# Kernel tuning notes

Measured on AMD Instinct MI355X. Metric: run time of the kernel, lower is better.

The kernel has to match this reference:

```python
import jax, jax.numpy as jnp
import numpy as np

B, L, N = 64, 64, 32           # programs, statement trees per program, nodes per tree
V, E, C, H, OUT = 100000, 128, 128, 100, 104
MAX_DEPTH = 10


def setup_inputs() -> dict:
    key = jax.random.key(0)
    ks = jax.random.split(key, 14)
    rng = np.random.default_rng(0)
    num_trees = B * L
    T = num_trees * N
    # random trees: parent index < node index, depth capped at MAX_DEPTH
    par = np.zeros((num_trees, N), np.int64)
    lev = np.zeros((num_trees, N), np.int64)
    for i in range(1, N):
        p = rng.integers(0, i, size=num_trees)
        pl = lev[np.arange(num_trees), p]
        too_deep = pl + 1 > MAX_DEPTH
        p = np.where(too_deep, 0, p)
        lev[:, i] = np.where(too_deep, 1, pl + 1)
        par[:, i] = p
    base = (np.arange(num_trees) * N)[:, None]
    parent = jnp.asarray((par + base).reshape(-1))          # global parent index
    level = jnp.asarray(lev.reshape(-1))
    tree_id = jnp.asarray(np.repeat(np.arange(num_trees), N))
    node_ids = jax.random.randint(ks[0], (T,), 0, V)
    r = lambda k, shape, s=0.05: (jax.random.normal(k, shape) * s).astype(jnp.float32)
    return {
        'node_ids': node_ids, 'parent': parent, 'level': level, 'tree_id': tree_id,
        'emb': r(ks[1], (V, E), 1.0),
        'W_lin': r(ks[2], (E, C)), 'b_lin': r(ks[3], (C,)),
        'w_ih_f': r(ks[4], (3 * H, C)), 'w_hh_f': r(ks[5], (3 * H, H)),
        'b_ih_f': r(ks[6], (3 * H,)), 'b_hh_f': r(ks[7], (3 * H,)),
        'w_ih_b': r(ks[8], (3 * H, C)), 'w_hh_b': r(ks[9], (3 * H, H)),
        'b_ih_b': r(ks[10], (3 * H,)), 'b_hh_b': r(ks[11], (3 * H,)),
        'fc_w': r(ks[12], (2 * H, OUT)), 'fc_b': r(ks[13], (OUT,)),
    }


def _run_gru(xs, wih, whh, bih, bhh, reverse):
    # xs: [L, B, C]; torch GRU gate math
    def step(hprev, x):
        gi = x @ wih.T + bih
        gh = hprev @ whh.T + bhh
        ir, iz, inn = jnp.split(gi, 3, axis=-1)
        hr, hz, hn = jnp.split(gh, 3, axis=-1)
        rg = jax.nn.sigmoid(ir + hr)
        zg = jax.nn.sigmoid(iz + hz)
        ng = jnp.tanh(inn + rg * hn)
        hnew = (1.0 - zg) * ng + zg * hprev
        return hnew, hnew
    h0 = jnp.zeros((xs.shape[1], whh.shape[1]), xs.dtype)
    _, out = jax.lax.scan(step, h0, xs, reverse=reverse)
    return out  # [L, B, H]


def _forward(node_ids, parent, level, tree_id, emb, W_lin, b_lin,
             w_ih_f, w_hh_f, b_ih_f, b_hh_f, w_ih_b, w_hh_b, b_ih_b, b_hh_b,
             fc_w, fc_b):
    # per-node: h = W*emb(id) + b, then child-sum bottom-up by depth level
    h = emb[node_ids] @ W_lin + b_lin            # [T, C]
    for d in range(MAX_DEPTH, 0, -1):
        contrib = jnp.where((level == d)[:, None], h, 0.0)
        h = h.at[parent].add(contrib)
    # per-tree max pool over all node hidden states -> statement vectors
    stmt = jax.ops.segment_max(h, tree_id, num_segments=B * L)  # [B*L, C]
    xs = stmt.reshape(B, L, C).transpose(1, 0, 2)               # [L, B, C]
    out_f = _run_gru(xs, w_ih_f, w_hh_f, b_ih_f, b_hh_f, reverse=False)
    out_b = _run_gru(xs, w_ih_b, w_hh_b, b_ih_b, b_hh_b, reverse=True)
    gru_out = jnp.concatenate([out_f, out_b], axis=-1)          # [L, B, 2H]
    pooled = gru_out.max(axis=0)                                # [B, 2H]
    return pooled @ fc_w + fc_b                                 # [B, OUT]


def reference(node_ids, parent, level, tree_id, emb, W_lin, b_lin,
              w_ih_f, w_hh_f, b_ih_f, b_hh_f, w_ih_b, w_hh_b, b_ih_b, b_hh_b,
              fc_w, fc_b):
    return _forward(node_ids, parent, level, tree_id, emb, W_lin, b_lin,
                    w_ih_f, w_hh_f, b_ih_f, b_hh_f, w_ih_b, w_hh_b, b_ih_b, b_hh_b,
                    fc_w, fc_b)
```

## Files before the change

kernel.cpp:

```cpp
#include <hip/hip_runtime.h>

typedef _Float16 half8 __attribute__((ext_vector_type(8)));
typedef float f32x4 __attribute__((ext_vector_type(4)));
typedef float f32x16 __attribute__((ext_vector_type(16)));

union H8 { half8 h; float4 f; };
union F4 { float4 f; f32x4 v; };

#define EDIM 128
#define CDIM 128
#define HDIM 100
#define ODIM 104

#define OFF_WFRAG  0u
#define OFF_WIH    32768u
#define OFF_WHH    229376u
#define OFF_BIASP  401408u
#define OFF_BHHN   404480u
#define OFF_STMT   405504u
#define OFF_GI     1454080u
#define OFF_POOL   14036992u

__device__ inline f32x4 zero4() { f32x4 z = {0.f, 0.f, 0.f, 0.f}; return z; }

__device__ inline float fast_exp2(float x) {
  float r; asm("v_exp_f32 %0, %1" : "=v"(r) : "v"(x)); return r;
}
__device__ inline float fast_rcp(float x) {
  float r; asm("v_rcp_f32 %0, %1" : "=v"(r) : "v"(x)); return r;
}
__device__ inline float sigmoid_f(float x) {
  return fast_rcp(1.f + fast_exp2(x * -1.44269504f));
}
__device__ inline float tanh_f(float x) {
  float e = fast_exp2(x * 2.88539008f);
  return fmaf(fast_rcp(1.f + e), -2.f, 1.f);
}

#define HSWZ(row) ((((row) & 3) << 4) ^ (((row) & 12) << 3))

__global__ __launch_bounds__(256) void astnn_prep(
    const float* __restrict__ W_lin,
    const float* __restrict__ wihf, const float* __restrict__ whhf,
    const float* __restrict__ bihf, const float* __restrict__ bhhf,
    const float* __restrict__ wihb, const float* __restrict__ whhb,
    const float* __restrict__ bihb, const float* __restrict__ bhhb,
    _Float16* __restrict__ wfrag, _Float16* __restrict__ wihfrag,
    _Float16* __restrict__ whhfrag, float* __restrict__ biasP)
{
  int gid = blockIdx.x * 256 + threadIdx.x;
  if (gid < 2048) {
    int i = gid, l = i & 63, kc = (i >> 6) & 3, nt = i >> 8;
    int n = (nt << 4) + (l & 15);
    int kb = (kc << 5) + ((l >> 4) << 3);
#pragma unroll
    for (int e = 0; e < 8; e++)
      wfrag[i * 8 + e] = (_Float16)W_lin[(kb + e) * CDIM + n];
  } else if (gid < 14336) {
    int i = gid - 2048, l = i & 63, kc = (i >> 6) & 7;
    int rest = i >> 9, nt = rest % 12, d = rest / 12;
    const float* wih = d ? wihb : wihf;
    int n = (nt << 5) + (l & 31), s = n >> 7, j = n & 127;
    int kb = (kc << 4) + ((l >> 5) << 3);
#pragma unroll
    for (int e = 0; e < 8; e++) {
      float v = (j < HDIM) ? wih[(s * HDIM + j) * CDIM + (kb + e)] : 0.f;
      wihfrag[i * 8 + e] = (_Float16)v;
    }
  } else if (gid < 25088) {
    int i = gid - 14336, l = i & 63, kc = (i >> 6) & 3;
    int rest = i >> 8, nt = rest % 21, d = rest / 21;
    const float* whh = d ? whhb : whhf;
    const float* bhh = d ? bhhb : bhhf;
    int n = (nt << 4) + (l & 15), s = n / 112, j = n - 112 * s;
    int kb = (kc << 5) + ((l >> 4) << 3);
#pragma unroll
    for (int e = 0; e < 8; e++) {
      int k = kb + e;
      float v = 0.f;
      if (j < HDIM) {
        if (k < HDIM) v = whh[(s * HDIM + j) * HDIM + k];
        else if (k == HDIM && s == 2) v = bhh[2 * HDIM + j];
      }
      whhfrag[i * 8 + e] = (_Float16)v;
    }
  } else if (gid < 25856) {
    int i = gid - 25088, d = i / 384, col = i % 384, s = col >> 7, j = col & 127;
    const float* bih = d ? bihb : bihf;
    const float* bhh = d ? bhhb : bhhf;
    float v = 0.f;
    if (j < HDIM) { v = bih[s * HDIM + j]; if (s < 2) v += bhh[s * HDIM + j]; }
    biasP[i] = v;
  }
}

__global__ __launch_bounds__(256, 2) void astnn_tree(
    const int* __restrict__ node_ids, const int* __restrict__ parent,
    const float* __restrict__ emb, const float* __restrict__ b_lin,
    const _Float16* __restrict__ wfrag, _Float16* __restrict__ stmt)
{
  __shared__ _Float16 ldsW[16384];
  __shared__ _Float16 ldsA[16384];
  __shared__ int ldsPar[128];
  __shared__ unsigned ldsAnc[128];

  const int t = threadIdx.x, blk = blockIdx.x;
  const int w = t >> 6, l = t & 63;
  const int base = blk * 128;

  if (t < 128) ldsPar[t] = parent[base + t] & 31;

  {
    const float4* wsrc = (const float4*)wfrag;
#pragma unroll
    for (int i = 0; i < 8; i++) ((float4*)ldsW)[i * 256 + t] = wsrc[i * 256 + t];
  }

  {
    const int r = t >> 1, hf = t & 1;
    const int nid = node_ids[base + r];
    const float4* erow = (const float4*)(emb + (size_t)nid * EDIM) + hf * 16;
#pragma unroll
    for (int b2 = 0; b2 < 2; b2++) {
      float4 stage[8];
#pragma unroll
      for (int i = 0; i < 8; i++) stage[i] = erow[b2 * 8 + i];
#pragma unroll
      for (int c4 = 0; c4 < 4; c4++) {
        H8 u;
#pragma unroll
        for (int e = 0; e < 8; e++)
          u.h[e] = (_Float16)(((const float*)&stage[0])[c4 * 8 + e]);
        int c = b2 * 4 + c4;
        int addr = (r * 256 + hf * 128 + c * 16) ^ ((r & 7) << 4);
        *(float4*)((char*)ldsA + addr) = u.f;
      }
    }
  }
  __syncthreads();

  if (t < 128) {
    int tree = t >> 5;
    unsigned mask = 0;
    int cur = t & 31;
#pragma unroll
    for (int it = 0; it < 11; ++it) { mask |= (1u << cur); cur = ldsPar[tree * 32 + cur]; }
    ldsAnc[t] = mask;
  }
  __syncthreads();

  f32x4 acc[2][8];
#pragma unroll
  for (int mt = 0; mt < 2; mt++)
#pragma unroll
    for (int nt = 0; nt < 8; nt++) acc[mt][nt] = zero4();
#pragma unroll
  for (int kc = 0; kc < 4; kc++) {
    half8 af[2];
#pragma unroll
    for (int mt = 0; mt < 2; mt++) {
      int row = (w * 2 + mt) * 16 + (l & 15);
      int addr = (row * 256 + (kc << 6) + ((l >> 4) << 4)) ^ ((row & 7) << 4);
      af[mt] = *(const half8*)((const char*)ldsA + addr);
    }
#pragma unroll
    for (int nt = 0; nt < 8; nt++) {
      half8 bf = *(const half8*)&ldsW[(((nt << 2) | kc) * 64 + l) * 8];
      acc[0][nt] = __builtin_amdgcn_mfma_f32_16x16x32_f16(af[0], bf, acc[0][nt], 0, 0, 0);
      acc[1][nt] = __builtin_amdgcn_mfma_f32_16x16x32_f16(af[1], bf, acc[1][nt], 0, 0, 0);
    }
  }
  __syncthreads();

#pragma unroll
  for (int mt = 0; mt < 2; mt++) {
    const int Mt = w * 2 + mt, tree = Mt >> 1, kc2 = Mt & 1;
#pragma unroll
    for (int nt = 0; nt < 8; nt++) {
      const float bl = b_lin[nt * 16 + (l & 15)];
      const int nt2 = nt >> 1;
      const int ncol = ((nt & 1) << 4) + (l & 15);
#pragma unroll
      for (int reg = 0; reg < 4; reg++) {
        int rowrem = ((l >> 4) << 2) + reg;
        int l2 = ((rowrem >> 3) << 5) + ncol;
        int idx = (((((tree << 2) + nt2) << 1) + kc2) * 64 + l2) * 8 + (rowrem & 7);
        ldsA[idx] = (_Float16)(acc[mt][nt][reg] + bl);
      }
    }
  }
  __syncthreads();

  {
    const int tree = w;
    half8 ancf[2];
#pragma unroll
    for (int kc2 = 0; kc2 < 2; kc2++) {
      H8 u;
#pragma unroll
      for (int e = 0; e < 8; e++) {
        int n = (kc2 << 4) + ((l >> 5) << 3) + e;
        unsigned m = ldsAnc[(tree << 5) + n];
        u.h[e] = (_Float16)(float)((m >> (l & 31)) & 1u);
      }
      ancf[kc2] = u.h;
    }
    f32x16 acc2[4];
#pragma unroll
    for (int nt2 = 0; nt2 < 4; nt2++)
#pragma unroll
      for (int e = 0; e < 16; e++) acc2[nt2][e] = 0.f;
#pragma unroll
    for (int nt2 = 0; nt2 < 4; nt2++)
#pragma unroll
      for (int kc2 = 0; kc2 < 2; kc2++) {
        half8 bf = *(const half8*)&ldsA[(((((tree << 2) + nt2) << 1) + kc2) * 64 + l) * 8];
        acc2[nt2] = __builtin_amdgcn_mfma_f32_32x32x16_f16(ancf[kc2], bf, acc2[nt2], 0, 0, 0);
      }
#pragma unroll
    for (int nt2 = 0; nt2 < 4; nt2++) {
      float m1 = acc2[nt2][0];
#pragma unroll
      for (int e = 1; e < 16; e++) m1 = fmaxf(m1, acc2[nt2][e]);
      m1 = fmaxf(m1, __shfl_xor(m1, 32));
      if (l < 32) {
        int g = blk * 4 + tree;
        int rowp = (g & 63) * 64 + (g >> 6);
        stmt[(size_t)rowp * CDIM + (nt2 << 5) + l] = (_Float16)m1;
      }
    }
  }
}

__global__ __launch_bounds__(256) void astnn_gi(
    const _Float16* __restrict__ stmt, const _Float16* __restrict__ wihfrag,
    const float* __restrict__ biasP, float* __restrict__ gi)
{
  __shared__ _Float16 ldsS[8192];
  const int tq = threadIdx.x, w = tq >> 6, l = tq & 63;
  const int tpos = blockIdx.x, dir = blockIdx.y;

  {
    const float4* src = (const float4*)(stmt + (size_t)tpos * 64 * CDIM);
#pragma unroll
    for (int i = 0; i < 4; i++) {
      int id = i * 256 + tq, row = id >> 4, ch = id & 15;
      float4 v = src[id];
      *(float4*)((char*)ldsS + ((row * 256 + ch * 16) ^ ((row & 7) << 4))) = v;
    }
  }
  half8 afr[3][8];
  {
    const half8* wf = (const half8*)wihfrag + dir * 6144;
#pragma unroll
    for (int i = 0; i < 3; i++) {
      int ct = w * 3 + i;
#pragma unroll
      for (int kc = 0; kc < 8; kc++) afr[i][kc] = wf[((ct << 3) + kc) * 64 + l];
    }
  }
  __syncthreads();

  f32x16 acc[2][3];
#pragma unroll
  for (int bt = 0; bt < 2; bt++)
#pragma unroll
    for (int i = 0; i < 3; i++)
#pragma unroll
      for (int e = 0; e < 16; e++) acc[bt][i][e] = 0.f;

#pragma unroll
  for (int kc = 0; kc < 8; kc++) {
    half8 bfr[2];
#pragma unroll
    for (int bt = 0; bt < 2; bt++) {
      int row = (bt << 5) + (l & 31);
      int kbyte = (kc << 5) + ((l >> 5) << 4);
      bfr[bt] = *(const half8*)((const char*)ldsS +
                                ((row * 256 + kbyte) ^ ((row & 7) << 4)));
    }
#pragma unroll
    for (int i = 0; i < 3; i++)
#pragma unroll
      for (int bt = 0; bt < 2; bt++)
        acc[bt][i] = __builtin_amdgcn_mfma_f32_32x32x16_f16(afr[i][kc], bfr[bt],
                                                            acc[bt][i], 0, 0, 0);
  }

  float* gout = gi + (((size_t)dir * 64 + tpos) * 384) * 64;
#pragma unroll
  for (int i = 0; i < 3; i++) {
#pragma unroll
    for (int reg = 0; reg < 16; reg++) {
      int rowfrag = (reg & 3) + ((reg >> 2) << 3) + ((l >> 5) << 2);
      int col = (w * 3 + i) * 32 + rowfrag;
      float bias = biasP[dir * 384 + col];
#pragma unroll
      for (int bt = 0; bt < 2; bt++)
        gout[(size_t)col * 64 + (bt << 5) + (l & 31)] = acc[bt][i][reg] + bias;
    }
  }
}

__global__ __launch_bounds__(448) void astnn_gru(
    const _Float16* __restrict__ whhfrag, const float* __restrict__ gi,
    float* __restrict__ pooled)
{
  __shared__ _Float16 hlds[4096];
  const int t = threadIdx.x, w = t >> 6, l = t & 63;
  const int mb = blockIdx.x, dir = blockIdx.y;
  for (int i = t; i < 512; i += 448)
    ((float4*)hlds)[i] = make_float4(0.f, 0.f, 0.f, 0.f);
  __syncthreads();
  if (t < 32) {
    int row = t & 15, buf = t >> 4;
    int addr = ((row * 256 + 200) ^ HSWZ(row)) + (buf << 12);
    *(_Float16*)((char*)hlds + addr) = (_Float16)1.0f;
  }

  const int j = (w << 4) + (l & 15);
  const bool jv = (j < HDIM);
  const int rloc = (l >> 4) << 2;
  const int grow = (mb << 4) + rloc;

  int raddr[4], waddr[4];
  {
    int row = l & 15;
#pragma unroll
    for (int kc = 0; kc < 4; kc++)
      raddr[kc] = (row * 256 + (kc << 6) + ((l >> 4) << 4)) ^ HSWZ(row);
#pragma unroll
    for (int reg = 0; reg < 4; reg++) {
      int rw = rloc + reg;
      waddr[reg] = (rw * 256 + (j << 1)) ^ HSWZ(rw);
    }
  }
  int loffB0 = (((0 << 7) + j) * 64 + grow) * 4;
  int loffB1 = (((1 << 7) + j) * 64 + grow) * 4;
  int loffB2 = (((2 << 7) + j) * 64 + grow) * 4;
  const char* gseq = (const char*)gi + (size_t)dir * 1572864 * 4;

  half8 bfr[3][4];
  {
    const half8* wf = (const half8*)whhfrag + dir * 5376;
#pragma unroll
    for (int s = 0; s < 3; s++)
#pragma unroll
      for (int kc = 0; kc < 4; kc++)
        bfr[s][kc] = wf[(((s * 7 + w) << 2) + kc) * 64 + l];
  }

  float hreg[4], pool[4];
#pragma unroll
  for (int i = 0; i < 4; i++) { hreg[i] = 0.f; pool[i] = -3.0e38f; }

  const ptrdiff_t dstep = (ptrdiff_t)(dir ? -24576 : 24576) * 4;
  const char* pbase = gseq + (size_t)(dir ? 63 : 0) * 24576 * 4;
  float4 gp[4][3];
#pragma unroll
  for (int d = 0; d < 4; d++) {
    const char* p = pbase + d * dstep;
    gp[d][0] = *(const float4*)(p + loffB0);
    gp[d][1] = *(const float4*)(p + loffB1);
    gp[d][2] = *(const float4*)(p + loffB2);
  }
  const char* ppre = pbase + 4 * dstep;
  __syncthreads();

#define GRU_BODY(U, ROFF, WOFF, PF)                                             \
  {                                                                             \
    F4 u0, u1; u0.f = gp[U][0]; u1.f = gp[U][1];                                \
    f32x4 acc0 = u0.v, acc1 = u1.v, acc2 = zero4();                             \
    float4 g2 = gp[U][2];                                                       \
    if (PF) {                                                                   \
      gp[U][0] = *(const float4*)(ppre + loffB0);                               \
      gp[U][1] = *(const float4*)(ppre + loffB1);                               \
      gp[U][2] = *(const float4*)(ppre + loffB2);                               \
      ppre += dstep;                                                            \
    }                                                                           \
    _Pragma("unroll")                                                           \
    for (int kc = 0; kc < 4; kc++) {                                            \
      half8 af = *(const half8*)((const char*)hlds + raddr[kc] + (ROFF));       \
      acc0 = __builtin_amdgcn_mfma_f32_16x16x32_f16(af, bfr[0][kc], acc0, 0, 0, 0); \
      acc1 = __builtin_amdgcn_mfma_f32_16x16x32_f16(af, bfr[1][kc], acc1, 0, 0, 0); \
      acc2 = __builtin_amdgcn_mfma_f32_16x16x32_f16(af, bfr[2][kc], acc2, 0, 0, 0); \
    }                                                                           \
    _Pragma("unroll")                                                           \
    for (int reg = 0; reg < 4; reg++) {                                         \
      float r = sigmoid_f(acc0[reg]);                                           \
      float z = sigmoid_f(acc1[reg]);                                           \
      float n = tanh_f(fmaf(r, acc2[reg], ((const float*)&g2)[reg]));           \
      float hn = n + z * (hreg[reg] - n);                                       \
      hreg[reg] = hn;                                                           \
      pool[reg] = fmaxf(pool[reg], hn);                                         \
      if (jv)                                                                   \
        *(_Float16*)((char*)hlds + waddr[reg] + (WOFF)) = (_Float16)hn;         \
    }                                                                           \
    asm volatile("s_waitcnt lgkmcnt(0)" ::: "memory");                          \
    __builtin_amdgcn_s_barrier();                                               \
    __builtin_amdgcn_sched_barrier(0);                                          \
  }

#pragma unroll 1
  for (int it = 0; it < 15; ++it) {
    GRU_BODY(0, 0, 4096, 1)
    GRU_BODY(1, 4096, 0, 1)
    GRU_BODY(2, 0, 4096, 1)
    GRU_BODY(3, 4096, 0, 1)
  }
  GRU_BODY(0, 0, 4096, 0)
  GRU_BODY(1, 4096, 0, 0)
  GRU_BODY(2, 0, 4096, 0)
  GRU_BODY(3, 4096, 0, 0)
#undef GRU_BODY

  if (jv) {
#pragma unroll
    for (int reg = 0; reg < 4; reg++)
      pooled[((size_t)dir << 13) + ((size_t)(grow + reg) << 7) + j] = pool[reg];
  }
}

__global__ __launch_bounds__(128) void astnn_fc(
    const float* __restrict__ pooled, const float* __restrict__ fc_w,
    const float* __restrict__ fc_b, float* __restrict__ out)
{
  __shared__ float p[200];
  const int b = blockIdx.x, t = threadIdx.x;
  for (int i = t; i < 200; i += 128) {
    int d = i / 100, jj = i - d * 100;
    p[i] = pooled[((size_t)d << 13) + (b << 7) + jj];
  }
  __syncthreads();
  if (t < ODIM) {
    float a = fc_b[t];
#pragma unroll 8
    for (int k = 0; k < 200; k++) a = fmaf(p[k], fc_w[k * ODIM + t], a);
    out[b * ODIM + t] = a;
  }
}

extern "C" void kernel_launch(void* const* d_in, const int* in_sizes, int n_in,
                              void* d_out, int out_size, void* d_ws, size_t ws_size,
                              hipStream_t stream)
{
  const int* node_ids = (const int*)d_in[0];
  const int* parent   = (const int*)d_in[1];
  const float* emb    = (const float*)d_in[4];
  const float* W_lin  = (const float*)d_in[5];
  const float* b_lin  = (const float*)d_in[6];
  const float* wihf   = (const float*)d_in[7];
  const float* whhf   = (const float*)d_in[8];
  const float* bihf   = (const float*)d_in[9];
  const float* bhhf   = (const float*)d_in[10];
  const float* wihb   = (const float*)d_in[11];
  const float* whhb   = (const float*)d_in[12];
  const float* bihb   = (const float*)d_in[13];
  const float* bhhb   = (const float*)d_in[14];
  const float* fc_w   = (const float*)d_in[15];
  const float* fc_b   = (const float*)d_in[16];

  char* ws = (char*)d_ws;
  _Float16* wfrag   = (_Float16*)(ws + OFF_WFRAG);
  _Float16* wihfrag = (_Float16*)(ws + OFF_WIH);
  _Float16* whhfrag = (_Float16*)(ws + OFF_WHH);
  float* biasP      = (float*)(ws + OFF_BIASP);
  _Float16* stmt    = (_Float16*)(ws + OFF_STMT);
  float* gi         = (float*)(ws + OFF_GI);
  float* pooled     = (float*)(ws + OFF_POOL);
  float* out        = (float*)d_out;

  astnn_prep<<<102, 256, 0, stream>>>(W_lin, wihf, whhf, bihf, bhhf,
                                      wihb, whhb, bihb, bhhb,
                                      wfrag, wihfrag, whhfrag, biasP);
  astnn_tree<<<1024, 256, 0, stream>>>(node_ids, parent, emb, b_lin, wfrag, stmt);
  astnn_gi<<<dim3(64, 2), 256, 0, stream>>>(stmt, wihfrag, biasP, gi);
  astnn_gru<<<dim3(4, 2), 448, 0, stream>>>(whhfrag, gi, pooled);
  astnn_fc<<<64, 128, 0, stream>>>(pooled, fc_w, fc_b, out);
}
```

Measured before the change: 85.57 us.

## Fuse GRU input projection into the recurrent GRU kernel

Removes the separate astnn_gi kernel that precomputed input gate activations for all timesteps into a large fp32 buffer. The GRU kernel now holds W_ih fragments in registers and computes the input projection per step with MFMA from prefetched fp16 statement vectors, and the prep kernel repacks W_ih into the same 16x16x32 fragment layout as W_hh. This drops one launch and the global write and read of the gi buffer. In exchange, the serial recurrent loop does roughly twice the MFMA work per step on only 8 blocks, though the input MFMAs do not depend on h and can overlap with the wait for it.

```diff
diff --git a/kernel.cpp b/kernel.cpp
--- a/kernel.cpp
+++ b/kernel.cpp
@@ -5,7 +5,6 @@
 typedef float f32x16 __attribute__((ext_vector_type(16)));
 
 union H8 { half8 h; float4 f; };
-union F4 { float4 f; f32x4 v; };
 
 #define EDIM 128
 #define CDIM 128
@@ -14,12 +13,10 @@
 
 #define OFF_WFRAG  0u
 #define OFF_WIH    32768u
-#define OFF_WHH    229376u
-#define OFF_BIASP  401408u
-#define OFF_BHHN   404480u
-#define OFF_STMT   405504u
-#define OFF_GI     1454080u
-#define OFF_POOL   14036992u
+#define OFF_WHH    204800u
+#define OFF_BIASP  376832u
+#define OFF_STMT   379904u
+#define OFF_POOL   1428480u
 
 __device__ inline f32x4 zero4() { f32x4 z = {0.f, 0.f, 0.f, 0.f}; return z; }
 
@@ -56,19 +53,20 @@
 #pragma unroll
     for (int e = 0; e < 8; e++)
       wfrag[i * 8 + e] = (_Float16)W_lin[(kb + e) * CDIM + n];
-  } else if (gid < 14336) {
-    int i = gid - 2048, l = i & 63, kc = (i >> 6) & 7;
-    int rest = i >> 9, nt = rest % 12, d = rest / 12;
+  } else if (gid < 12800) {
+    int i = gid - 2048, l = i & 63, kc = (i >> 6) & 3;
+    int rest = i >> 8, nt = rest % 21, d = rest / 21;
     const float* wih = d ? wihb : wihf;
-    int n = (nt << 5) + (l & 31), s = n >> 7, j = n & 127;
-    int kb = (kc << 4) + ((l >> 5) << 3);
+    int n = (nt << 4) + (l & 15), s = n / 112, j = n - 112 * s;
+    int kb = (kc << 5) + ((l >> 4) << 3);
 #pragma unroll
     for (int e = 0; e < 8; e++) {
-      float v = (j < HDIM) ? wih[(s * HDIM + j) * CDIM + (kb + e)] : 0.f;
+      int k = kb + e;
+      float v = (j < HDIM) ? wih[(s * HDIM + j) * CDIM + k] : 0.f;
       wihfrag[i * 8 + e] = (_Float16)v;
     }
-  } else if (gid < 25088) {
-    int i = gid - 14336, l = i & 63, kc = (i >> 6) & 3;
+  } else if (gid < 23552) {
+    int i = gid - 12800, l = i & 63, kc = (i >> 6) & 3;
     int rest = i >> 8, nt = rest % 21, d = rest / 21;
     const float* whh = d ? whhb : whhf;
     const float* bhh = d ? bhhb : bhhf;
@@ -84,8 +82,8 @@
       }
       whhfrag[i * 8 + e] = (_Float16)v;
     }
-  } else if (gid < 25856) {
-    int i = gid - 25088, d = i / 384, col = i % 384, s = col >> 7, j = col & 127;
+  } else if (gid < 24320) {
+    int i = gid - 23552, d = i / 384, col = i % 384, s = col >> 7, j = col & 127;
     const float* bih = d ? bihb : bihf;
     const float* bhh = d ? bhhb : bhhf;
     float v = 0.f;
@@ -232,78 +230,9 @@
   }
 }
 
-__global__ __launch_bounds__(256) void astnn_gi(
-    const _Float16* __restrict__ stmt, const _Float16* __restrict__ wihfrag,
-    const float* __restrict__ biasP, float* __restrict__ gi)
-{
-  __shared__ _Float16 ldsS[8192];
-  const int tq = threadIdx.x, w = tq >> 6, l = tq & 63;
-  const int tpos = blockIdx.x, dir = blockIdx.y;
-
-  {
-    const float4* src = (const float4*)(stmt + (size_t)tpos * 64 * CDIM);
-#pragma unroll
-    for (int i = 0; i < 4; i++) {
-      int id = i * 256 + tq, row = id >> 4, ch = id & 15;
-      float4 v = src[id];
-      *(float4*)((char*)ldsS + ((row * 256 + ch * 16) ^ ((row & 7) << 4))) = v;
-    }
-  }
-  half8 afr[3][8];
-  {
-    const half8* wf = (const half8*)wihfrag + dir * 6144;
-#pragma unroll
-    for (int i = 0; i < 3; i++) {
-      int ct = w * 3 + i;
-#pragma unroll
-      for (int kc = 0; kc < 8; kc++) afr[i][kc] = wf[((ct << 3) + kc) * 64 + l];
-    }
-  }
-  __syncthreads();
-
-  f32x16 acc[2][3];
-#pragma unroll
-  for (int bt = 0; bt < 2; bt++)
-#pragma unroll
-    for (int i = 0; i < 3; i++)
-#pragma unroll
-      for (int e = 0; e < 16; e++) acc[bt][i][e] = 0.f;
-
-#pragma unroll
-  for (int kc = 0; kc < 8; kc++) {
-    half8 bfr[2];
-#pragma unroll
-    for (int bt = 0; bt < 2; bt++) {
-      int row = (bt << 5) + (l & 31);
-      int kbyte = (kc << 5) + ((l >> 5) << 4);
-      bfr[bt] = *(const half8*)((const char*)ldsS +
-                                ((row * 256 + kbyte) ^ ((row & 7) << 4)));
-    }
-#pragma unroll
-    for (int i = 0; i < 3; i++)
-#pragma unroll
-      for (int bt = 0; bt < 2; bt++)
-        acc[bt][i] = __builtin_amdgcn_mfma_f32_32x32x16_f16(afr[i][kc], bfr[bt],
-                                                            acc[bt][i], 0, 0, 0);
-  }
-
-  float* gout = gi + (((size_t)dir * 64 + tpos) * 384) * 64;
-#pragma unroll
-  for (int i = 0; i < 3; i++) {
-#pragma unroll
-    for (int reg = 0; reg < 16; reg++) {
-      int rowfrag = (reg & 3) + ((reg >> 2) << 3) + ((l >> 5) << 2);
-      int col = (w * 3 + i) * 32 + rowfrag;
-      float bias = biasP[dir * 384 + col];
-#pragma unroll
-      for (int bt = 0; bt < 2; bt++)
-        gout[(size_t)col * 64 + (bt << 5) + (l & 31)] = acc[bt][i][reg] + bias;
-    }
-  }
-}
-
 __global__ __launch_bounds__(448) void astnn_gru(
-    const _Float16* __restrict__ whhfrag, const float* __restrict__ gi,
+    const _Float16* __restrict__ whhfrag, const _Float16* __restrict__ wihfrag,
+    const _Float16* __restrict__ stmt, const float* __restrict__ biasP,
     float* __restrict__ pooled)
 {
   __shared__ _Float16 hlds[4096];
@@ -335,61 +264,78 @@
       waddr[reg] = (rw * 256 + (j << 1)) ^ HSWZ(rw);
     }
   }
-  int loffB0 = (((0 << 7) + j) * 64 + grow) * 4;
-  int loffB1 = (((1 << 7) + j) * 64 + grow) * 4;
-  int loffB2 = (((2 << 7) + j) * 64 + grow) * 4;
-  const char* gseq = (const char*)gi + (size_t)dir * 1572864 * 4;
-
-  half8 bfr[3][4];
+
+  half8 bfr[3][4], bfw[3][4];
   {
-    const half8* wf = (const half8*)whhfrag + dir * 5376;
+    const half8* wfh = (const half8*)whhfrag + dir * 5376;
+    const half8* wfi = (const half8*)wihfrag + dir * 5376;
 #pragma unroll
     for (int s = 0; s < 3; s++)
 #pragma unroll
-      for (int kc = 0; kc < 4; kc++)
-        bfr[s][kc] = wf[(((s * 7 + w) << 2) + kc) * 64 + l];
-  }
+      for (int kc = 0; kc < 4; kc++) {
+        int idx = (((s * 7 + w) << 2) + kc) * 64 + l;
+        bfr[s][kc] = wfh[idx];
+        bfw[s][kc] = wfi[idx];
+      }
+  }
+  const float bias0 = biasP[dir * 384 + j];
+  const float bias1 = biasP[dir * 384 + 128 + j];
+  const float bias2 = biasP[dir * 384 + 256 + j];
+
+  int soff[4];
+#pragma unroll
+  for (int kc = 0; kc < 4; kc++)
+    soff[kc] = (((mb << 4) + (l & 15)) * 256) + (kc << 6) + ((l >> 4) << 4);
+  const ptrdiff_t sstep = dir ? -16384 : 16384;
+  const char* sbase = (const char*)stmt + (size_t)(dir ? 63 : 0) * 16384;
+
+  half8 sf0[4], sf1[4];
+#pragma unroll
+  for (int kc = 0; kc < 4; kc++) sf0[kc] = *(const half8*)(sbase + soff[kc]);
+  const char* spre = sbase + sstep;
+#pragma unroll
+  for (int kc = 0; kc < 4; kc++) sf1[kc] = *(const half8*)(spre + soff[kc]);
+  spre += sstep;
 
   float hreg[4], pool[4];
 #pragma unroll
   for (int i = 0; i < 4; i++) { hreg[i] = 0.f; pool[i] = -3.0e38f; }
-
-  const ptrdiff_t dstep = (ptrdiff_t)(dir ? -24576 : 24576) * 4;
-  const char* pbase = gseq + (size_t)(dir ? 63 : 0) * 24576 * 4;
-  float4 gp[4][3];
-#pragma unroll
-  for (int d = 0; d < 4; d++) {
-    const char* p = pbase + d * dstep;
-    gp[d][0] = *(const float4*)(p + loffB0);
-    gp[d][1] = *(const float4*)(p + loffB1);
-    gp[d][2] = *(const float4*)(p + loffB2);
-  }
-  const char* ppre = pbase + 4 * dstep;
-  __syncthreads();
-
-#define GRU_BODY(U, ROFF, WOFF, PF)                                             \
+  __syncthreads();
+
+#define GRU_BODY(SF, ROFF, WOFF, PF)                                            \
   {                                                                             \
-    F4 u0, u1; u0.f = gp[U][0]; u1.f = gp[U][1];                                \
-    f32x4 acc0 = u0.v, acc1 = u1.v, acc2 = zero4();                             \
-    float4 g2 = gp[U][2];                                                       \
+    half8 afh[4];                                                               \
+    _Pragma("unroll")                                                           \
+    for (int kc = 0; kc < 4; kc++)                                              \
+      afh[kc] = *(const half8*)((const char*)hlds + raddr[kc] + (ROFF));        \
+    f32x4 acc0 = {bias0, bias0, bias0, bias0};                                  \
+    f32x4 acc1 = {bias1, bias1, bias1, bias1};                                  \
+    f32x4 acc2i = {bias2, bias2, bias2, bias2};                                 \
+    f32x4 acc2h = zero4();                                                      \
+    _Pragma("unroll")                                                           \
+    for (int kc = 0; kc < 4; kc++) {      \
+      acc0  = __builtin_amdgcn_mfma_f32_16x16x32_f16(SF[kc], bfw[0][kc], acc0, 0, 0, 0);  \
+      acc1  = __builtin_amdgcn_mfma_f32_16x16x32_f16(SF[kc], bfw[1][kc], acc1, 0, 0, 0);  \
+      acc2i = __builtin_amdgcn_mfma_f32_16x16x32_f16(SF[kc], bfw[2][kc], acc2i, 0, 0, 0); \
+    }                                                                           \
     if (PF) {                                                                   \
-      gp[U][0] = *(const float4*)(ppre + loffB0);                               \
-      gp[U][1] = *(const float4*)(ppre + loffB1);                               \
-      gp[U][2] = *(const float4*)(ppre + loffB2);                               \
-      ppre += dstep;                                                            \
+      SF[0] = *(const half8*)(spre + soff[0]);                                  \
+      SF[1] = *(const half8*)(spre + soff[1]);                                  \
+      SF[2] = *(const half8*)(spre + soff[2]);                                  \
+      SF[3] = *(const half8*)(spre + soff[3]);                                  \
+      spre += sstep;                                                            \
     }                                                                           \
     _Pragma("unroll")                                                           \
     for (int kc = 0; kc < 4; kc++) {                                            \
-      half8 af = *(const half8*)((const char*)hlds + raddr[kc] + (ROFF));       \
-      acc0 = __builtin_amdgcn_mfma_f32_16x16x32_f16(af, bfr[0][kc], acc0, 0, 0, 0); \
-      acc1 = __builtin_amdgcn_mfma_f32_16x16x32_f16(af, bfr[1][kc], acc1, 0, 0, 0); \
-      acc2 = __builtin_amdgcn_mfma_f32_16x16x32_f16(af, bfr[2][kc], acc2, 0, 0, 0); \
+      acc0  = __builtin_amdgcn_mfma_f32_16x16x32_f16(afh[kc], bfr[0][kc], acc0, 0, 0, 0); \
+      acc1  = __builtin_amdgcn_mfma_f32_16x16x32_f16(afh[kc], bfr[1][kc], acc1, 0, 0, 0); \
+      acc2h = __builtin_amdgcn_mfma_f32_16x16x32_f16(afh[kc], bfr[2][kc], acc2h, 0, 0, 0);\
     }                                                                           \
     _Pragma("unroll")                                                           \
     for (int reg = 0; reg < 4; reg++) {                                         \
       float r = sigmoid_f(acc0[reg]);                                           \
       float z = sigmoid_f(acc1[reg]);                                           \
-      float n = tanh_f(fmaf(r, acc2[reg], ((const float*)&g2)[reg]));           \
+      float n = tanh_f(fmaf(r, acc2h[reg], acc2i[reg]));                        \
       float hn = n + z * (hreg[reg] - n);                                       \
       hreg[reg] = hn;                                                           \
       pool[reg] = fmaxf(pool[reg], hn);                                         \
@@ -402,16 +348,12 @@
   }
 
 #pragma unroll 1
-  for (int it = 0; it < 15; ++it) {
-    GRU_BODY(0, 0, 4096, 1)
-    GRU_BODY(1, 4096, 0, 1)
-    GRU_BODY(2, 0, 4096, 1)
-    GRU_BODY(3, 4096, 0, 1)
-  }
-  GRU_BODY(0, 0, 4096, 0)
-  GRU_BODY(1, 4096, 0, 0)
-  GRU_BODY(2, 0, 4096, 0)
-  GRU_BODY(3, 4096, 0, 0)
+  for (int it = 0; it < 31; ++it) {
+    GRU_BODY(sf0, 0, 4096, 1)
+    GRU_BODY(sf1, 4096, 0, 1)
+  }
+  GRU_BODY(sf0, 0, 4096, 0)
+  GRU_BODY(sf1, 4096, 0, 0)
 #undef GRU_BODY
 
   if (jv) {
@@ -466,15 +408,13 @@
   _Float16* whhfrag = (_Float16*)(ws + OFF_WHH);
   float* biasP      = (float*)(ws + OFF_BIASP);
   _Float16* stmt    = (_Float16*)(ws + OFF_STMT);
-  float* gi         = (float*)(ws + OFF_GI);
   float* pooled     = (float*)(ws + OFF_POOL);
   float* out        = (float*)d_out;
 
-  astnn_prep<<<102, 256, 0, stream>>>(W_lin, wihf, whhf, bihf, bhhf,
-                                      wihb, whhb, bihb, bhhb,
-                                      wfrag, wihfrag, whhfrag, biasP);
+  astnn_prep<<<95, 256, 0, stream>>>(W_lin, wihf, whhf, bihf, bhhf,
+                                     wihb, whhb, bihb, bhhb,
+                                     wfrag, wihfrag, whhfrag, biasP);
   astnn_tree<<<1024, 256, 0, stream>>>(node_ids, parent, emb, b_lin, wfrag, stmt);
-  astnn_gi<<<dim3(64, 2), 256, 0, stream>>>(stmt, wihfrag, biasP, gi);
-  astnn_gru<<<dim3(4, 2), 448, 0, stream>>>(whhfrag, gi, pooled);
+  astnn_gru<<<dim3(4, 2), 448, 0, stream>>>(whhfrag, wihfrag, stmt, biasP, pooled);
   astnn_fc<<<64, 128, 0, stream>>>(pooled, fc_w, fc_b, out);
 }
```

Measured after the change: 97.26 us. 1.14x slower.
